# Performance work log

Measured on AMD Instinct MI355X. Metric: run time of the kernel, lower is better.

Reference implementation:

```python
import jax, jax.numpy as jnp
import numpy as np
import math

B, S, D, H = 8, 1024, 1024, 16
HD = D // H  # head_features = 64
SCALE = math.sqrt(HD)


def setup_inputs() -> dict:
    key = jax.random.key(0)
    k0, k1, k2, k3, k4 = jax.random.split(key, 5)
    x = jax.random.normal(k0, (B, S, D), dtype=jnp.float32)
    attn_mask = (jax.random.uniform(k1, (B, S, S)) < 0.9).astype(jnp.float32)
    w_scale = 1.0 / math.sqrt(D)  # keep unsafe exp in finite range
    Wq = jax.random.normal(k2, (D, D), dtype=jnp.float32) * w_scale
    Wk = jax.random.normal(k3, (D, D), dtype=jnp.float32) * w_scale
    Wv = jax.random.normal(k4, (D, D), dtype=jnp.float32) * w_scale
    return {"x": x, "attn_mask": attn_mask, "Wq": Wq, "Wk": Wk, "Wv": Wv}


def reference(x, attn_mask, Wq, Wk, Wv):
    b, s, _ = x.shape

    def split_heads(t):  # [b,s,D] -> [b,H,s,HD]
        return t.reshape(b, s, H, HD).transpose(0, 2, 1, 3)

    q = split_heads(x @ Wq)
    k = split_heads(x @ Wk)
    v = split_heads(x @ Wv)

    # unsafe softmax: exp without max subtraction, multiplicative mask, +1e-8 denom
    scores = jnp.einsum('bhsd,bhtd->bhst', q, k) / SCALE
    e = jnp.exp(scores) * attn_mask[:, None, :, :]
    w = e / (e.sum(axis=3, keepdims=True) + 1e-8)

    ctx = jnp.einsum('bhst,bhtd->bhsd', w, v)  # [b,H,s,HD]
    return ctx.transpose(0, 2, 1, 3).reshape(b, s, D)
```

## Files before the change

### kernel.cpp

```cpp
#include <hip/hip_runtime.h>

#define KDIM 1024

typedef _Float16 half8 __attribute__((ext_vector_type(8)));
typedef _Float16 half4 __attribute__((ext_vector_type(4)));
typedef __fp16 fp16x2 __attribute__((ext_vector_type(2)));
typedef __fp16 fp16x4 __attribute__((ext_vector_type(4)));
typedef float f32x4 __attribute__((ext_vector_type(4)));

#if defined(__has_builtin)
#if __has_builtin(__builtin_amdgcn_global_load_lds)
#define HAVE_GLDS 1
#endif
#if __has_builtin(__builtin_amdgcn_exp2f)
#define EXP2(x) __builtin_amdgcn_exp2f(x)
#endif
#if __has_builtin(__builtin_amdgcn_cvt_pkrtz)
#define HAVE_PKRTZ 1
#endif
#if __has_builtin(__builtin_amdgcn_fdot2)
#define HAVE_FDOT2 1
#endif
#endif
#ifndef EXP2
#define EXP2(x) exp2f(x)
#endif

__device__ __forceinline__ void stage16(const _Float16* g, _Float16* wave_base, int lane) {
#ifdef HAVE_GLDS
  __builtin_amdgcn_global_load_lds(
      (const __attribute__((address_space(1))) void*)g,
      (__attribute__((address_space(3))) void*)wave_base, 16, 0, 0);
#else
  *(half8*)(wave_base + lane * 8) = *(const half8*)g;
#endif
}

__global__ void prep_kernel(const float* __restrict__ x, const float* __restrict__ am,
                            const float* __restrict__ Wq, const float* __restrict__ Wk,
                            const float* __restrict__ Wv, _Float16* __restrict__ xb,
                            _Float16* __restrict__ Wqkvt, unsigned long long* __restrict__ bits) {
  __shared__ _Float16 tile[32][33];
  int bid = blockIdx.x;
  if (bid < 8192) {
    size_t i = ((size_t)bid * 256 + threadIdx.x) * 4;
    float4 v = *(const float4*)(x + i);
    half4 h = { (_Float16)v.x, (_Float16)v.y, (_Float16)v.z, (_Float16)v.w };
    *(half4*)(xb + i) = h;
  } else if (bid < 11264) {
    int zz = bid - 8192;
    int z = zz >> 10;
    int rem = zz & 1023;
    int bx = rem & 31, by = rem >> 5;
    const float* src = z == 0 ? Wq : (z == 1 ? Wk : Wv);
    _Float16* dst = Wqkvt + (size_t)z * KDIM * KDIM;
    float sc = (z == 0) ? 0.18033688011112042f : 1.0f;
    int tx = threadIdx.x & 31, ty = threadIdx.x >> 5;
    int c0 = bx * 32, r0 = by * 32;
#pragma unroll
    for (int i = 0; i < 4; i++) {
      int r = r0 + ty + i * 8;
      tile[tx][ty + i * 8] = (_Float16)(src[(size_t)r * KDIM + c0 + tx] * sc);
    }
    __syncthreads();
#pragma unroll
    for (int i = 0; i < 4; i++) {
      int n = c0 + ty + i * 8;
      dst[(size_t)n * KDIM + r0 + tx] = tile[ty + i * 8][tx];
    }
  } else {
    size_t i = (size_t)(bid - 11264) * 256 + threadIdx.x;
    unsigned long long b = __ballot(am[i] != 0.0f);
    if ((threadIdx.x & 63) == 0) bits[i >> 6] = b;
  }
}

__global__ __launch_bounds__(256, 2)
void gemm_kernel(const _Float16* __restrict__ A, const _Float16* __restrict__ Bt,
                 _Float16* __restrict__ Qt, _Float16* __restrict__ Kh,
                 _Float16* __restrict__ Vth) {
  __shared__ _Float16 As[128 * 32];
  __shared__ _Float16 Bs[128 * 32];
  int tid = threadIdx.x;
  int lane = tid & 63, w4 = tid >> 6;
  int la = lane & 15, qd = lane >> 4;
  int wm = w4 & 1, wn = w4 >> 1;
  int m0 = blockIdx.y * 128, n0 = blockIdx.x * 128;
  int r = tid >> 2, c = (tid & 3) * 8;
  const _Float16* Ag = A + (size_t)(m0 + r) * KDIM + c;
  const _Float16* Bg = Bt + (size_t)(n0 + r) * KDIM + c;
  _Float16* a0 = As + w4 * 512;
  _Float16* b0 = Bs + w4 * 512;
  f32x4 acc[4][4] = {};
  for (int kt = 0; kt < KDIM; kt += 32) {
    stage16(Ag + kt, a0, lane);
    stage16(Ag + (size_t)64 * KDIM + kt, a0 + 2048, lane);
    stage16(Bg + kt, b0, lane);
    stage16(Bg + (size_t)64 * KDIM + kt, b0 + 2048, lane);
    __syncthreads();
    half8 af[4], bf[4];
#pragma unroll
    for (int mi = 0; mi < 4; mi++)
      af[mi] = *(const half8*)(As + (wm * 64 + mi * 16 + la) * 32 + qd * 8);
#pragma unroll
    for (int ni = 0; ni < 4; ni++)
      bf[ni] = *(const half8*)(Bs + (wn * 64 + ni * 16 + la) * 32 + qd * 8);
#pragma unroll
    for (int mi = 0; mi < 4; mi++)
#pragma unroll
      for (int ni = 0; ni < 4; ni++)
        acc[mi][ni] = __builtin_amdgcn_mfma_f32_16x16x32_f16(af[mi], bf[ni], acc[mi][ni], 0, 0, 0);
    __syncthreads();
  }
  int which = n0 >> 10;
  int hh = ((n0 + wn * 64) >> 6) & 15;
  int mbase = m0 + wm * 64;
  int b = mbase >> 10, s0 = mbase & 1023;
  if (which == 1) {
#pragma unroll
    for (int mi = 0; mi < 4; mi++)
#pragma unroll
      for (int ni = 0; ni < 4; ni++) {
        f32x4 v = acc[mi][ni];
        int s = s0 + mi * 16 + qd * 4;
        int d = ni * 16 + la;
#pragma unroll
        for (int rg = 0; rg < 4; rg++)
          Kh[(((size_t)(b * 16 + hh)) * 1024 + s + rg) * 64 + d] = (_Float16)v[rg];
      }
  } else {
    _Float16* dst = (which == 0) ? Qt : Vth;
    _Float16* ep = (w4 < 2) ? (As + w4 * 2048) : (Bs + (w4 - 2) * 2048);
    _Float16* base = dst + ((size_t)(b * 16 + hh)) * 64 * 1024;
    int rr = lane >> 2, c4 = lane & 3;
#pragma unroll
    for (int ni = 0; ni < 4; ni++) {
#pragma unroll
      for (int mi = 0; mi < 4; mi++) {
        f32x4 v = acc[mi][ni];
        half4 hv = { (_Float16)v[0], (_Float16)v[1], (_Float16)v[2], (_Float16)v[3] };
        *(half4*)(ep + la * 72 + mi * 16 + qd * 4) = hv;
      }
      half8 o0 = *(const half8*)(ep + rr * 72 + c4 * 16);
      half8 o1 = *(const half8*)(ep + rr * 72 + c4 * 16 + 8);
      _Float16* gp = base + (size_t)(ni * 16 + rr) * 1024 + s0 + c4 * 16;
      *(half8*)gp = o0;
      *(half8*)(gp + 8) = o1;
    }
  }
}

__global__ __launch_bounds__(512, 2)
void attn_kernel(const _Float16* __restrict__ Qt, const _Float16* __restrict__ K,
                 const _Float16* __restrict__ Vt, const unsigned long long* __restrict__ mbits,
                 float* __restrict__ out) {
  __shared__ _Float16 Ks[2][2 * 64 * 32];
  __shared__ _Float16 Vs[2][2 * 64 * 40];
  int tid = threadIdx.x;
  int lane = tid & 63, w4 = tid >> 6;
  int la = lane & 15, qd = lane >> 4;
  int linear = blockIdx.x;
  int xlo = linear & 7;
  int tmp = linear >> 3;
  int qt = tmp & 3;
  int hb = (tmp >> 2) * 8 + xlo;
  int h = hb & 15, b = hb >> 4;
  const _Float16* Qp = Qt + (size_t)hb * 64 * 1024;
  const _Float16* Kp = K + (size_t)hb * 1024 * 64;
  const _Float16* Vp = Vt + (size_t)hb * 64 * 1024;
  int q0w = qt * 256 + w4 * 16;
  half8 qf[2][2];
#pragma unroll
  for (int qi = 0; qi < 2; qi++)
#pragma unroll
    for (int ks = 0; ks < 2; ks++)
#pragma unroll
      for (int j = 0; j < 8; j++)
        qf[qi][ks][j] = Qp[(size_t)(ks * 32 + qd * 8 + j) * 1024 + q0w + qi * 128 + la];
  unsigned long long mq[2][4];
#pragma unroll
  for (int qi = 0; qi < 2; qi++) {
    const ulonglong2* mp =
        (const ulonglong2*)(mbits + ((size_t)b * 1024 + q0w + qi * 128 + la) * 16 + qd * 4);
    ulonglong2 m01 = mp[0];
    ulonglong2 m23 = mp[1];
    mq[qi][0] = m01.x; mq[qi][1] = m01.y; mq[qi][2] = m23.x; mq[qi][3] = m23.y;
  }
  f32x4 acco[2][4] = {};
  float rs[2] = {0.f, 0.f};
  int kt_t = (tid & 255) >> 2;
  int kt_d = (tid >> 8) * 32 + (tid & 3) * 8;
  int vd = tid >> 3;
  int vt = (tid & 7) * 8;
  int vs_off = (vt >= 32 ? 2560 : 0) + vd * 40 + (vt & 31);
#if defined(HAVE_FDOT2) && defined(HAVE_PKRTZ)
  fp16x2 one2 = { (__fp16)1.0f, (__fp16)1.0f };
#endif
  {
    stage16(Kp + (size_t)kt_t * 64 + kt_d, Ks[0] + w4 * 512, lane);
    half8 vv = *(const half8*)(Vp + (size_t)vd * 1024 + vt);
    *(half8*)(Vs[0] + vs_off) = vv;
  }
  __syncthreads();
  for (int tt = 0; tt < 16; tt++) {
    int cur = tt & 1, nxt = cur ^ 1;
    half8 vvn;
    if (tt < 15) {
      vvn = *(const half8*)(Vp + (size_t)vd * 1024 + (tt + 1) * 64 + vt);
      stage16(Kp + (size_t)((tt + 1) * 64 + kt_t) * 64 + kt_d, Ks[nxt] + w4 * 512, lane);
    }
    const _Float16* ks_ = Ks[cur];
    const _Float16* vs_ = Vs[cur];
    unsigned long long mw0 = __shfl(mq[0][tt & 3], ((tt >> 2) << 4) + la);
    unsigned long long mw1 = __shfl(mq[1][tt & 3], ((tt >> 2) << 4) + la);
#pragma unroll
    for (int tsub = 0; tsub < 4; tsub++) {
      half8 kf0 = *(const half8*)(ks_ + (tsub * 16 + la) * 32 + qd * 8);
      half8 kf1 = *(const half8*)(ks_ + 2048 + (tsub * 16 + la) * 32 + qd * 8);
      f32x4 a0 = {}, a1 = {};
      a0 = __builtin_amdgcn_mfma_f32_16x16x32_f16(kf0, qf[0][0], a0, 0, 0, 0);
      a1 = __builtin_amdgcn_mfma_f32_16x16x32_f16(kf0, qf[1][0], a1, 0, 0, 0);
      a0 = __builtin_amdgcn_mfma_f32_16x16x32_f16(kf1, qf[0][1], a0, 0, 0, 0);
      a1 = __builtin_amdgcn_mfma_f32_16x16x32_f16(kf1, qf[1][1], a1, 0, 0, 0);
      half4 pf[2];
#pragma unroll
      for (int qi = 0; qi < 2; qi++) {
        const f32x4& aa = qi ? a1 : a0;
        unsigned long long mw = qi ? mw1 : mw0;
        float e0 = ((mw >> (tsub * 16 + qd * 4 + 0)) & 1ull) ? EXP2(aa[0]) : 0.0f;
        float e1 = ((mw >> (tsub * 16 + qd * 4 + 1)) & 1ull) ? EXP2(aa[1]) : 0.0f;
        float e2 = ((mw >> (tsub * 16 + qd * 4 + 2)) & 1ull) ? EXP2(aa[2]) : 0.0f;
        float e3 = ((mw >> (tsub * 16 + qd * 4 + 3)) & 1ull) ? EXP2(aa[3]) : 0.0f;
#ifdef HAVE_PKRTZ
        fp16x2 p01 = __builtin_amdgcn_cvt_pkrtz(e0, e1);
        fp16x2 p23 = __builtin_amdgcn_cvt_pkrtz(e2, e3);
        fp16x4 pfv = __builtin_shufflevector(p01, p23, 0, 1, 2, 3);
        pf[qi] = __builtin_bit_cast(half4, pfv);
#else
        pf[qi][0] = (_Float16)e0; pf[qi][1] = (_Float16)e1;
        pf[qi][2] = (_Float16)e2; pf[qi][3] = (_Float16)e3;
#endif
#if defined(HAVE_FDOT2) && defined(HAVE_PKRTZ)
        rs[qi] = __builtin_amdgcn_fdot2(p01, one2, rs[qi], false);
        rs[qi] = __builtin_amdgcn_fdot2(p23, one2, rs[qi], false);
#else
        rs[qi] += e0 + e1 + e2 + e3;
#endif
      }
#pragma unroll
      for (int nsub = 0; nsub < 4; nsub++) {
        half4 vf = *(const half4*)(vs_ + (tsub >> 1) * 2560 + (nsub * 16 + la) * 40 +
                                   (tsub & 1) * 16 + qd * 4);
        acco[0][nsub] = __builtin_amdgcn_mfma_f32_16x16x16f16(pf[0], vf, acco[0][nsub], 0, 0, 0);
        acco[1][nsub] = __builtin_amdgcn_mfma_f32_16x16x16f16(pf[1], vf, acco[1][nsub], 0, 0, 0);
      }
    }
    if (tt < 15) *(half8*)(Vs[nxt] + vs_off) = vvn;
    __syncthreads();
  }
  float* op = out + (size_t)b * 1024 * 1024 + (size_t)h * 64;
#pragma unroll
  for (int qi = 0; qi < 2; qi++) {
    float r0 = rs[qi];
    r0 += __shfl_xor(r0, 16);
    r0 += __shfl_xor(r0, 32);
    float inv_q = 1.0f / (r0 + 1e-8f);
#pragma unroll
    for (int rg = 0; rg < 4; rg++) {
      float inv = __shfl(inv_q, qd * 4 + rg);
      int s = q0w + qi * 128 + qd * 4 + rg;
#pragma unroll
      for (int nsub = 0; nsub < 4; nsub++)
        op[(size_t)s * 1024 + nsub * 16 + la] = acco[qi][nsub][rg] * inv;
    }
  }
}

extern "C" void kernel_launch(void* const* d_in, const int* in_sizes, int n_in,
                              void* d_out, int out_size, void* d_ws, size_t ws_size,
                              hipStream_t stream) {
  (void)in_sizes; (void)n_in; (void)out_size; (void)ws_size;
  const float* x = (const float*)d_in[0];
  const float* am = (const float*)d_in[1];
  const float* Wq = (const float*)d_in[2];
  const float* Wk = (const float*)d_in[3];
  const float* Wv = (const float*)d_in[4];
  float* out = (float*)d_out;

  char* p = (char*)d_ws;
  _Float16* xb = (_Float16*)p;    p += (size_t)8192 * 1024 * 2;
  _Float16* Wqkvt = (_Float16*)p; p += (size_t)3 * 1024 * 1024 * 2;
  _Float16* Qt = (_Float16*)p;    p += (size_t)8192 * 1024 * 2;
  _Float16* Kh = (_Float16*)p;    p += (size_t)8192 * 1024 * 2;
  _Float16* Vth = (_Float16*)p;   p += (size_t)8192 * 1024 * 2;
  unsigned long long* mb = (unsigned long long*)p;

  prep_kernel<<<44032, 256, 0, stream>>>(x, am, Wq, Wk, Wv, xb, Wqkvt, mb);
  gemm_kernel<<<dim3(24, 64), 256, 0, stream>>>(xb, Wqkvt, Qt, Kh, Vth);
  attn_kernel<<<512, 512, 0, stream>>>(Qt, Kh, Vth, mb, out);
}
```

Before: 260.9 us.

## Restructure QKV GEMM into 256x256 tiles with double-buffered swizzled LDS pipeline

Replaces the 128x128, BK=32 QKV projection GEMM with 256x256 tiles, 8 waves, BK=64, and double-buffered LDS. Global-to-LDS loads for the next K step are interleaved with four MFMA quadrants under explicit vmcnt/lgkmcnt waits and barriers. Rows are XOR-swizzled to avoid bank conflicts, MFMA sections are raised in priority, and the grid is remapped for better L2 locality. This targets the load stalls and low arithmetic intensity of the old single-buffered loop. It costs more LDS and registers per block, and 384 blocks may leave the machine unevenly loaded.

```diff
diff --git a/kernel.cpp b/kernel.cpp
--- a/kernel.cpp
+++ b/kernel.cpp
@@ -35,6 +35,17 @@
   *(half8*)(wave_base + lane * 8) = *(const half8*)g;
 #endif
 }
+
+#define BARRIER() __builtin_amdgcn_s_barrier()
+#define LGKM0()                                         \
+  do {                                                  \
+    asm volatile("s_waitcnt lgkmcnt(0)" ::: "memory");  \
+    __builtin_amdgcn_sched_barrier(0);                  \
+  } while (0)
+#define VMCNT(n)                                               \
+  do {                                                         \
+    asm volatile("s_waitcnt vmcnt(" #n ")" ::: "memory");      \
+  } while (0)
 
 __global__ void prep_kernel(const float* __restrict__ x, const float* __restrict__ am,
                             const float* __restrict__ Wq, const float* __restrict__ Wk,
@@ -75,77 +86,169 @@
   }
 }
 
-__global__ __launch_bounds__(256, 2)
+template <int MH, int NH>
+__device__ __forceinline__ void mfma_quad(f32x4 (&acc)[8][4], const half8 (&af)[4][2],
+                                          const half8 (&bf)[2][2]) {
+  __builtin_amdgcn_s_setprio(1);
+#pragma unroll
+  for (int mi = 0; mi < 4; ++mi)
+#pragma unroll
+    for (int nj = 0; nj < 2; ++nj) {
+      acc[MH * 4 + mi][NH * 2 + nj] = __builtin_amdgcn_mfma_f32_16x16x32_f16(
+          af[mi][0], bf[nj][0], acc[MH * 4 + mi][NH * 2 + nj], 0, 0, 0);
+      acc[MH * 4 + mi][NH * 2 + nj] = __builtin_amdgcn_mfma_f32_16x16x32_f16(
+          af[mi][1], bf[nj][1], acc[MH * 4 + mi][NH * 2 + nj], 0, 0, 0);
+    }
+  __builtin_amdgcn_s_setprio(0);
+}
+
+__global__ __launch_bounds__(512, 2)
 void gemm_kernel(const _Float16* __restrict__ A, const _Float16* __restrict__ Bt,
                  _Float16* __restrict__ Qt, _Float16* __restrict__ Kh,
                  _Float16* __restrict__ Vth) {
-  __shared__ _Float16 As[128 * 32];
-  __shared__ _Float16 Bs[128 * 32];
+  __shared__ _Float16 As[2 * 16384];
+  __shared__ _Float16 Bs[2 * 16384];
   int tid = threadIdx.x;
-  int lane = tid & 63, w4 = tid >> 6;
+  int lane = tid & 63, w = tid >> 6;
   int la = lane & 15, qd = lane >> 4;
-  int wm = w4 & 1, wn = w4 >> 1;
-  int m0 = blockIdx.y * 128, n0 = blockIdx.x * 128;
-  int r = tid >> 2, c = (tid & 3) * 8;
-  const _Float16* Ag = A + (size_t)(m0 + r) * KDIM + c;
-  const _Float16* Bg = Bt + (size_t)(n0 + r) * KDIM + c;
-  _Float16* a0 = As + w4 * 512;
-  _Float16* b0 = Bs + w4 * 512;
-  f32x4 acc[4][4] = {};
-  for (int kt = 0; kt < KDIM; kt += 32) {
-    stage16(Ag + kt, a0, lane);
-    stage16(Ag + (size_t)64 * KDIM + kt, a0 + 2048, lane);
-    stage16(Bg + kt, b0, lane);
-    stage16(Bg + (size_t)64 * KDIM + kt, b0 + 2048, lane);
-    __syncthreads();
-    half8 af[4], bf[4];
-#pragma unroll
-    for (int mi = 0; mi < 4; mi++)
-      af[mi] = *(const half8*)(As + (wm * 64 + mi * 16 + la) * 32 + qd * 8);
-#pragma unroll
-    for (int ni = 0; ni < 4; ni++)
-      bf[ni] = *(const half8*)(Bs + (wn * 64 + ni * 16 + la) * 32 + qd * 8);
-#pragma unroll
-    for (int mi = 0; mi < 4; mi++)
-#pragma unroll
-      for (int ni = 0; ni < 4; ni++)
-        acc[mi][ni] = __builtin_amdgcn_mfma_f32_16x16x32_f16(af[mi], bf[ni], acc[mi][ni], 0, 0, 0);
-    __syncthreads();
-  }
+  int wm = w & 1, wn = w >> 1;
+  int bid = blockIdx.x;
+  int wg = (bid & 7) * 48 + (bid >> 3);
+  int by = wg / 12, bx = wg - by * 12;
+  int m0 = by * 256, n0 = bx * 256;
+  int srow = tid >> 3;
+  int scc = ((srow & 7) ^ (tid & 7)) << 3;
+  const int rc0 = ((qd ^ (la & 7)) << 3);
+  const int rc1 = (((4 | qd) ^ (la & 7)) << 3);
+
+  const _Float16* Ab = A + (size_t)m0 * KDIM;
+  const _Float16* Bb = Bt + (size_t)n0 * KDIM;
+
+  auto stA = [&](int buf, int h, int kt) {
+#pragma unroll
+    for (int l = 0; l < 2; ++l) {
+      int r = h * 128 + srow + l * 64;
+      stage16(Ab + (size_t)r * KDIM + kt + scc,
+              As + buf * 16384 + h * 8192 + l * 4096 + w * 512, lane);
+    }
+  };
+  auto stB = [&](int buf, int h, int kt) {
+#pragma unroll
+    for (int l = 0; l < 2; ++l) {
+      int r = h * 128 + srow + l * 64;
+      stage16(Bb + (size_t)r * KDIM + kt + scc,
+              Bs + buf * 16384 + h * 8192 + l * 4096 + w * 512, lane);
+    }
+  };
+
+  f32x4 acc[8][4] = {};
+  half8 af[4][2], bf[2][2];
+
+  auto ldAf = [&](int buf, int mh) {
+#pragma unroll
+    for (int mi = 0; mi < 4; ++mi) {
+      const _Float16* p = As + buf * 16384 + mh * 8192 + (wm * 64 + mi * 16 + la) * 64;
+      af[mi][0] = *(const half8*)(p + rc0);
+      af[mi][1] = *(const half8*)(p + rc1);
+    }
+  };
+  auto ldBf = [&](int buf, int nh) {
+#pragma unroll
+    for (int nj = 0; nj < 2; ++nj) {
+      const _Float16* p = Bs + buf * 16384 + nh * 8192 + (wn * 32 + nj * 16 + la) * 64;
+      bf[nj][0] = *(const half8*)(p + rc0);
+      bf[nj][1] = *(const half8*)(p + rc1);
+    }
+  };
+
+  stA(0, 0, 0); stA(0, 1, 0); stB(0, 0, 0); stB(0, 1, 0);
+  stA(1, 0, 64); stB(1, 0, 64);
+  VMCNT(4);
+  BARRIER();
+
+  for (int t = 0; t < 16; ++t) {
+    int cur = t & 1, nxt = cur ^ 1;
+    int k1 = (t + 1) << 6, k2 = (t + 2) << 6;
+    ldAf(cur, 0);
+    ldBf(cur, 0);
+    if (t < 15) stA(nxt, 1, k1);
+    BARRIER();
+    LGKM0();
+    mfma_quad<0, 0>(acc, af, bf);
+    BARRIER();
+    ldBf(cur, 1);
+    if (t < 15) stB(nxt, 1, k1);
+    BARRIER();
+    LGKM0();
+    mfma_quad<0, 1>(acc, af, bf);
+    BARRIER();
+    ldAf(cur, 1);
+    ldBf(cur, 0);
+    if (t < 14) stA(cur, 0, k2);
+    BARRIER();
+    LGKM0();
+    mfma_quad<1, 0>(acc, af, bf);
+    BARRIER();
+    ldBf(cur, 1);
+    if (t < 14) stB(cur, 0, k2);
+    BARRIER();
+    LGKM0();
+    mfma_quad<1, 1>(acc, af, bf);
+    if (t < 14) { VMCNT(4); } else { VMCNT(0); }
+    BARRIER();
+  }
+
   int which = n0 >> 10;
-  int hh = ((n0 + wn * 64) >> 6) & 15;
-  int mbase = m0 + wm * 64;
-  int b = mbase >> 10, s0 = mbase & 1023;
+  int n0k = n0 & 1023;
   if (which == 1) {
 #pragma unroll
-    for (int mi = 0; mi < 4; mi++)
-#pragma unroll
-      for (int ni = 0; ni < 4; ni++) {
-        f32x4 v = acc[mi][ni];
-        int s = s0 + mi * 16 + qd * 4;
-        int d = ni * 16 + la;
-#pragma unroll
-        for (int rg = 0; rg < 4; rg++)
-          Kh[(((size_t)(b * 16 + hh)) * 1024 + s + rg) * 64 + d] = (_Float16)v[rg];
-      }
+    for (int mh = 0; mh < 2; ++mh) {
+      int srow0 = m0 + mh * 128 + wm * 64;
+      int b = srow0 >> 10, s0 = srow0 & 1023;
+#pragma unroll
+      for (int nh = 0; nh < 2; ++nh)
+#pragma unroll
+        for (int nj = 0; nj < 2; ++nj) {
+          int colh = n0k + nh * 128 + wn * 32 + nj * 16;
+          int hh = colh >> 6;
+          int d = (colh & 63) + la;
+          _Float16* kb = Kh + (size_t)(b * 16 + hh) * 1024 * 64;
+#pragma unroll
+          for (int mi = 0; mi < 4; ++mi) {
+            f32x4 v = acc[mh * 4 + mi][nh * 2 + nj];
+            int s = s0 + mi * 16 + qd * 4;
+#pragma unroll
+            for (int rg = 0; rg < 4; ++rg)
+              kb[(size_t)(s + rg) * 64 + d] = (_Float16)v[rg];
+          }
+        }
+    }
   } else {
     _Float16* dst = (which == 0) ? Qt : Vth;
-    _Float16* ep = (w4 < 2) ? (As + w4 * 2048) : (Bs + (w4 - 2) * 2048);
-    _Float16* base = dst + ((size_t)(b * 16 + hh)) * 64 * 1024;
+    _Float16* ep = As + w * 1280;
     int rr = lane >> 2, c4 = lane & 3;
 #pragma unroll
-    for (int ni = 0; ni < 4; ni++) {
-#pragma unroll
-      for (int mi = 0; mi < 4; mi++) {
-        f32x4 v = acc[mi][ni];
-        half4 hv = { (_Float16)v[0], (_Float16)v[1], (_Float16)v[2], (_Float16)v[3] };
-        *(half4*)(ep + la * 72 + mi * 16 + qd * 4) = hv;
-      }
-      half8 o0 = *(const half8*)(ep + rr * 72 + c4 * 16);
-      half8 o1 = *(const half8*)(ep + rr * 72 + c4 * 16 + 8);
-      _Float16* gp = base + (size_t)(ni * 16 + rr) * 1024 + s0 + c4 * 16;
-      *(half8*)gp = o0;
-      *(half8*)(gp + 8) = o1;
+    for (int mh = 0; mh < 2; ++mh) {
+      int srow0 = m0 + mh * 128 + wm * 64;
+      int b = srow0 >> 10, s0 = srow0 & 1023;
+#pragma unroll
+      for (int nh = 0; nh < 2; ++nh)
+#pragma unroll
+        for (int nj = 0; nj < 2; ++nj) {
+          int colh = n0k + nh * 128 + wn * 32 + nj * 16;
+          int hh = colh >> 6, d0 = colh & 63;
+#pragma unroll
+          for (int mi = 0; mi < 4; ++mi) {
+            f32x4 v = acc[mh * 4 + mi][nh * 2 + nj];
+            half4 hv = { (_Float16)v[0], (_Float16)v[1], (_Float16)v[2], (_Float16)v[3] };
+            *(half4*)(ep + la * 72 + mi * 16 + qd * 4) = hv;
+          }
+          half8 o0 = *(const half8*)(ep + rr * 72 + c4 * 16);
+          half8 o1 = *(const half8*)(ep + rr * 72 + c4 * 16 + 8);
+          _Float16* gp = dst + ((size_t)(b * 16 + hh) * 64 + d0 + rr) * 1024 + s0 + c4 * 16;
+          *(half8*)gp = o0;
+          *(half8*)(gp + 8) = o1;
+        }
     }
   }
 }
@@ -296,6 +399,6 @@
   unsigned long long* mb = (unsigned long long*)p;
 
   prep_kernel<<<44032, 256, 0, stream>>>(x, am, Wq, Wk, Wv, xb, Wqkvt, mb);
-  gemm_kernel<<<dim3(24, 64), 256, 0, stream>>>(xb, Wqkvt, Qt, Kh, Vth);
+  gemm_kernel<<<dim3(384), 512, 0, stream>>>(xb, Wqkvt, Qt, Kh, Vth);
   attn_kernel<<<512, 512, 0, stream>>>(Qt, Kh, Vth, mb, out);
 }
```

Result: no change. 259.6 us (-0.5%).
